# Performance work log

Measured on AMD Instinct MI355X. Metric: run time of the kernel, lower is better.

The kernel has to match this reference:

```python
import jax, jax.numpy as jnp
import numpy as np

N_NODES = 100000
INPUT_DIM = 512
OUTPUT_DIM = 128
N_EDGES = 300000


def setup_inputs() -> dict:
    key = jax.random.key(0)
    k1, k2, k3, k4, k5 = jax.random.split(key, 5)
    x = jax.random.normal(k1, (N_NODES, INPUT_DIM), dtype=jnp.float32)
    train_edges = jax.random.randint(k2, (N_EDGES, 2), 0, N_NODES, dtype=jnp.int64)
    train_false_edges = jax.random.randint(k3, (N_EDGES, 2), 0, N_NODES, dtype=jnp.int64)
    # learned params (xavier / kaiming init approximated with uniform fan-based scales)
    limit_w = float(np.sqrt(6.0 / (INPUT_DIM + OUTPUT_DIM)))
    weight = jax.random.uniform(k4, (INPUT_DIM, OUTPUT_DIM), dtype=jnp.float32,
                                minval=-limit_w, maxval=limit_w)
    limit_w3 = float(np.sqrt(6.0 / OUTPUT_DIM) / np.sqrt(2.0))
    weight_three = jax.random.uniform(k5, (OUTPUT_DIM, 1), dtype=jnp.float32,
                                      minval=-limit_w3, maxval=limit_w3)
    return {"x": x, "train_edges": train_edges, "train_false_edges": train_false_edges,
            "weight": weight, "weight_three": weight_three}


def _decode(z, edges, weight_three):
    # gather endpoints, elementwise multiply, matvec against weight_three
    prod = z[edges[:, 0]] * z[edges[:, 1]]  # [E, output_dim]
    return prod @ weight_three               # [E, 1]


def reference(x, train_edges, train_false_edges, weight, weight_three):
    z = x @ weight  # encode: [N, output_dim]
    z1 = _decode(z, train_edges, weight_three)
    z2 = _decode(z, train_false_edges, weight_three)
    return jax.nn.sigmoid(jnp.concatenate((z1, z2), axis=0))
```

## Files before the change

kernel.cpp:

```cpp
#include <hip/hip_runtime.h>
#include <math.h>

#define IN_DIM 512
#define OUT_DIM 128
#define BM 64
#define BK 64
#define NKT (IN_DIM / BK)

typedef __attribute__((ext_vector_type(8))) __bf16 bf16x8;
typedef __attribute__((ext_vector_type(4))) float f32x4;

__device__ inline unsigned short f2bf(float f) {
    unsigned u = __float_as_uint(f);
    u += 0x7FFFu + ((u >> 16) & 1u);
    return (unsigned short)(u >> 16);
}
__device__ inline float bf2f(unsigned short h) {
    return __uint_as_float((unsigned)h << 16);
}
__device__ inline unsigned pack2(unsigned short a, unsigned short b) {
    return (unsigned)a | ((unsigned)b << 16);
}

__device__ inline int swz(int row, int kbyte) {
    return row * 128 + (kbyte ^ ((row & 7) << 4));
}

__global__ void wt2_kernel(const float* __restrict__ w, unsigned short* __restrict__ wt2) {
    int idx = blockIdx.x * 256 + threadIdx.x;
    int k = idx >> 7;
    int n = idx & 127;
    wt2[(((k >> 3) * 128) + n) * 8 + (k & 7)] = f2bf(w[idx]);
}

__global__ __launch_bounds__(256, 4) void gemm_mfma(const float* __restrict__ x,
                                                    const unsigned short* __restrict__ wt2,
                                                    unsigned short* __restrict__ zb,
                                                    int M) {
    __shared__ unsigned short sAh[BM * BK];
    __shared__ unsigned short sAl[BM * BK];
    char* const pAh = (char*)sAh;
    char* const pAl = (char*)sAl;

    const int tid  = threadIdx.x;
    const int lane = tid & 63;
    const int wid  = tid >> 6;
    const int wm   = wid >> 1;
    const int wn   = wid & 1;
    const int block_row = blockIdx.x * BM;

    f32x4 acc[2][4];
#pragma unroll
    for (int i = 0; i < 2; ++i)
#pragma unroll
        for (int j = 0; j < 4; ++j) acc[i][j] = (f32x4){0.f, 0.f, 0.f, 0.f};

    const int a_row = tid >> 2;
    const int a_col = (tid & 3) * 16;
    const bool a_ok = (block_row + a_row) < M;
    const float* xp = x + (size_t)(block_row + a_row) * IN_DIM + a_col;
    const int a_b0 = swz(a_row, a_col * 2);
    const int a_b1 = swz(a_row, a_col * 2 + 16);

    const int fr  = lane & 15;
    const int fk4 = lane >> 4;
    const int fkb = fk4 * 16;

    const unsigned short* wtb = wt2 + (size_t)fk4 * 1024 + (wn * 64 + fr) * 8;

    float4 ra[4];
    const float4 z4 = make_float4(0.f, 0.f, 0.f, 0.f);

#pragma unroll
    for (int i = 0; i < 4; ++i) ra[i] = a_ok ? *(const float4*)(xp + 4 * i) : z4;

#pragma unroll
    for (int kt = 0; kt < NKT; ++kt) {
        if (kt) __syncthreads();
        unsigned short h[16], l[16];
        const float* rf = (const float*)ra;
#pragma unroll
        for (int i = 0; i < 16; ++i) {
            h[i] = f2bf(rf[i]);
            l[i] = f2bf(rf[i] - bf2f(h[i]));
        }
        uint4 uh0, uh1, ul0, ul1;
        uh0.x = pack2(h[0], h[1]);  uh0.y = pack2(h[2], h[3]);
        uh0.z = pack2(h[4], h[5]);  uh0.w = pack2(h[6], h[7]);
        uh1.x = pack2(h[8], h[9]);  uh1.y = pack2(h[10], h[11]);
        uh1.z = pack2(h[12], h[13]); uh1.w = pack2(h[14], h[15]);
        ul0.x = pack2(l[0], l[1]);  ul0.y = pack2(l[2], l[3]);
        ul0.z = pack2(l[4], l[5]);  ul0.w = pack2(l[6], l[7]);
        ul1.x = pack2(l[8], l[9]);  ul1.y = pack2(l[10], l[11]);
        ul1.z = pack2(l[12], l[13]); ul1.w = pack2(l[14], l[15]);
        *(uint4*)(pAh + a_b0) = uh0;
        *(uint4*)(pAh + a_b1) = uh1;
        *(uint4*)(pAl + a_b0) = ul0;
        *(uint4*)(pAl + a_b1) = ul1;
        __syncthreads();

        if (kt + 1 < NKT) {
            const int k0 = (kt + 1) * BK;
#pragma unroll
            for (int i = 0; i < 4; ++i)
                ra[i] = a_ok ? *(const float4*)(xp + k0 + 4 * i) : z4;
        }

#pragma unroll
        for (int ks = 0; ks < 2; ++ks) {
            bf16x8 ah[2], al[2], bv[4];
#pragma unroll
            for (int mf = 0; mf < 2; ++mf) {
                ah[mf] = *(const bf16x8*)(pAh + swz(wm * 32 + mf * 16 + fr, ks * 64 + fkb));
                al[mf] = *(const bf16x8*)(pAl + swz(wm * 32 + mf * 16 + fr, ks * 64 + fkb));
            }
#pragma unroll
            for (int nf = 0; nf < 4; ++nf)
                bv[nf] = *(const bf16x8*)(wtb + kt * 8192 + ks * 4096 + nf * 128);
#pragma unroll
            for (int mf = 0; mf < 2; ++mf)
#pragma unroll
                for (int nf = 0; nf < 4; ++nf) {
                    acc[mf][nf] = __builtin_amdgcn_mfma_f32_16x16x32_bf16(
                        ah[mf], bv[nf], acc[mf][nf], 0, 0, 0);
                    acc[mf][nf] = __builtin_amdgcn_mfma_f32_16x16x32_bf16(
                        al[mf], bv[nf], acc[mf][nf], 0, 0, 0);
                }
        }
    }

    const int crow0 = (lane >> 4) * 4;
    const int ccol  = lane & 15;
#pragma unroll
    for (int mf = 0; mf < 2; ++mf)
#pragma unroll
        for (int r = 0; r < 4; ++r) {
            const int grow = block_row + wm * 32 + mf * 16 + crow0 + r;
            if (grow < M) {
                unsigned short* zr = zb + (size_t)grow * OUT_DIM + wn * 64 + ccol;
#pragma unroll
                for (int nf = 0; nf < 4; ++nf)
                    zr[nf * 16] = f2bf(acc[mf][nf][r]);
            }
        }
}

__global__ __launch_bounds__(256) void decode_kernel(const unsigned short* __restrict__ zb,
                                                     const int* __restrict__ e1,
                                                     const int* __restrict__ e2,
                                                     const float* __restrict__ w3,
                                                     float* __restrict__ out,
                                                     int E1, int E2) {
    const int tid  = threadIdx.x;
    const int lane = tid & 63;
    const int sub  = lane & 15;
    const int sg   = lane >> 4;
    const int Etot = E1 + E2;
    const int nquads = (Etot + 3) >> 2;

    float w3r[8];
    *(float4*)&w3r[0] = *(const float4*)(w3 + sub * 8);
    *(float4*)&w3r[4] = *(const float4*)(w3 + sub * 8 + 4);

    const int wave_global = blockIdx.x * 4 + (tid >> 6);
    const int nwaves = gridDim.x * 4;

    for (int q = wave_global; q < nquads; q += nwaves) {
        const int e = q * 4 + sg;
        if (e < Etot) {
            int2 ab;
            if (e < E1) ab = ((const int2*)e1)[e];
            else        ab = ((const int2*)e2)[e - E1];

            const uint4 ua = *(const uint4*)(zb + (size_t)ab.x * OUT_DIM + sub * 8);
            const uint4 ub = *(const uint4*)(zb + (size_t)ab.y * OUT_DIM + sub * 8);
            const unsigned pa[4] = {ua.x, ua.y, ua.z, ua.w};
            const unsigned pb[4] = {ub.x, ub.y, ub.z, ub.w};

            float v = 0.f;
#pragma unroll
            for (int i = 0; i < 4; ++i) {
                const float a0 = __uint_as_float(pa[i] << 16);
                const float a1 = __uint_as_float(pa[i] & 0xFFFF0000u);
                const float b0 = __uint_as_float(pb[i] << 16);
                const float b1 = __uint_as_float(pb[i] & 0xFFFF0000u);
                v = fmaf(a0 * b0, w3r[2 * i], v);
                v = fmaf(a1 * b1, w3r[2 * i + 1], v);
            }

            v += __shfl_xor(v, 8);
            v += __shfl_xor(v, 4);
            v += __shfl_xor(v, 2);
            v += __shfl_xor(v, 1);

            if (sub == 0) out[e] = 1.f / (1.f + __expf(-v));
        }
    }
}

extern "C" void kernel_launch(void* const* d_in, const int* in_sizes, int n_in,
                              void* d_out, int out_size, void* d_ws, size_t ws_size,
                              hipStream_t stream) {
    const float* x  = (const float*)d_in[0];
    const int*   e1 = (const int*)d_in[1];
    const int*   e2 = (const int*)d_in[2];
    const float* w  = (const float*)d_in[3];
    const float* w3 = (const float*)d_in[4];

    float* out = (float*)d_out;

    const int M  = in_sizes[0] / IN_DIM;
    const int E1 = in_sizes[1] / 2;
    const int E2 = in_sizes[2] / 2;

    unsigned short* zbuf = (unsigned short*)d_ws;
    unsigned short* wt2  = zbuf + (size_t)M * OUT_DIM;

    wt2_kernel<<<(IN_DIM * OUT_DIM) / 256, 256, 0, stream>>>(w, wt2);
    gemm_mfma<<<(M + BM - 1) / BM, 256, 0, stream>>>(x, wt2, zbuf, M);
    decode_kernel<<<4096, 256, 0, stream>>>(zbuf, e1, e2, w3, out, E1, E2);
}
```

Before: 102.7 us.

## Drop split-bf16 low part of x in encoder GEMM and pack decode math

```diff
diff --git a/kernel.cpp b/kernel.cpp
--- a/kernel.cpp
+++ b/kernel.cpp
@@ -9,17 +9,15 @@
 
 typedef __attribute__((ext_vector_type(8))) __bf16 bf16x8;
 typedef __attribute__((ext_vector_type(4))) float f32x4;
+typedef __attribute__((ext_vector_type(2))) float f32x2;
 
 __device__ inline unsigned short f2bf(float f) {
     unsigned u = __float_as_uint(f);
     u += 0x7FFFu + ((u >> 16) & 1u);
     return (unsigned short)(u >> 16);
 }
-__device__ inline float bf2f(unsigned short h) {
-    return __uint_as_float((unsigned)h << 16);
-}
-__device__ inline unsigned pack2(unsigned short a, unsigned short b) {
-    return (unsigned)a | ((unsigned)b << 16);
+__device__ inline unsigned pack2f(float a, float b) {
+    return (unsigned)f2bf(a) | ((unsigned)f2bf(b) << 16);
 }
 
 __device__ inline int swz(int row, int kbyte) {
@@ -33,14 +31,12 @@
     wt2[(((k >> 3) * 128) + n) * 8 + (k & 7)] = f2bf(w[idx]);
 }
 
-__global__ __launch_bounds__(256, 4) void gemm_mfma(const float* __restrict__ x,
+__global__ __launch_bounds__(256, 6) void gemm_mfma(const float* __restrict__ x,
                                                     const unsigned short* __restrict__ wt2,
                                                     unsigned short* __restrict__ zb,
                                                     int M) {
-    __shared__ unsigned short sAh[BM * BK];
-    __shared__ unsigned short sAl[BM * BK];
-    char* const pAh = (char*)sAh;
-    char* const pAl = (char*)sAl;
+    __shared__ unsigned short sA[BM * BK];
+    char* const pA = (char*)sA;
 
     const int tid  = threadIdx.x;
     const int lane = tid & 63;
@@ -77,26 +73,14 @@
 #pragma unroll
     for (int kt = 0; kt < NKT; ++kt) {
         if (kt) __syncthreads();
-        unsigned short h[16], l[16];
         const float* rf = (const float*)ra;
-#pragma unroll
-        for (int i = 0; i < 16; ++i) {
-            h[i] = f2bf(rf[i]);
-            l[i] = f2bf(rf[i] - bf2f(h[i]));
-        }
-        uint4 uh0, uh1, ul0, ul1;
-        uh0.x = pack2(h[0], h[1]);  uh0.y = pack2(h[2], h[3]);
-        uh0.z = pack2(h[4], h[5]);  uh0.w = pack2(h[6], h[7]);
-        uh1.x = pack2(h[8], h[9]);  uh1.y = pack2(h[10], h[11]);
-        uh1.z = pack2(h[12], h[13]); uh1.w = pack2(h[14], h[15]);
-        ul0.x = pack2(l[0], l[1]);  ul0.y = pack2(l[2], l[3]);
-        ul0.z = pack2(l[4], l[5]);  ul0.w = pack2(l[6], l[7]);
-        ul1.x = pack2(l[8], l[9]);  ul1.y = pack2(l[10], l[11]);
-        ul1.z = pack2(l[12], l[13]); ul1.w = pack2(l[14], l[15]);
-        *(uint4*)(pAh + a_b0) = uh0;
-        *(uint4*)(pAh + a_b1) = uh1;
-        *(uint4*)(pAl + a_b0) = ul0;
-        *(uint4*)(pAl + a_b1) = ul1;
+        uint4 u0, u1;
+        u0.x = pack2f(rf[0], rf[1]);   u0.y = pack2f(rf[2], rf[3]);
+        u0.z = pack2f(rf[4], rf[5]);   u0.w = pack2f(rf[6], rf[7]);
+        u1.x = pack2f(rf[8], rf[9]);   u1.y = pack2f(rf[10], rf[11]);
+        u1.z = pack2f(rf[12], rf[13]); u1.w = pack2f(rf[14], rf[15]);
+        *(uint4*)(pA + a_b0) = u0;
+        *(uint4*)(pA + a_b1) = u1;
         __syncthreads();
 
         if (kt + 1 < NKT) {
@@ -108,24 +92,19 @@
 
 #pragma unroll
         for (int ks = 0; ks < 2; ++ks) {
-            bf16x8 ah[2], al[2], bv[4];
-#pragma unroll
-            for (int mf = 0; mf < 2; ++mf) {
-                ah[mf] = *(const bf16x8*)(pAh + swz(wm * 32 + mf * 16 + fr, ks * 64 + fkb));
-                al[mf] = *(const bf16x8*)(pAl + swz(wm * 32 + mf * 16 + fr, ks * 64 + fkb));
-            }
+            bf16x8 af[2], bv[4];
+#pragma unroll
+            for (int mf = 0; mf < 2; ++mf)
+                af[mf] = *(const bf16x8*)(pA + swz(wm * 32 + mf * 16 + fr, ks * 64 + fkb));
 #pragma unroll
             for (int nf = 0; nf < 4; ++nf)
                 bv[nf] = *(const bf16x8*)(wtb + kt * 8192 + ks * 4096 + nf * 128);
 #pragma unroll
             for (int mf = 0; mf < 2; ++mf)
 #pragma unroll
-                for (int nf = 0; nf < 4; ++nf) {
+                for (int nf = 0; nf < 4; ++nf)
                     acc[mf][nf] = __builtin_amdgcn_mfma_f32_16x16x32_bf16(
-                        ah[mf], bv[nf], acc[mf][nf], 0, 0, 0);
-                    acc[mf][nf] = __builtin_amdgcn_mfma_f32_16x16x32_bf16(
-                        al[mf], bv[nf], acc[mf][nf], 0, 0, 0);
-                }
+                        af[mf], bv[nf], acc[mf][nf], 0, 0, 0);
         }
     }
 
@@ -158,9 +137,15 @@
     const int Etot = E1 + E2;
     const int nquads = (Etot + 3) >> 2;
 
-    float w3r[8];
-    *(float4*)&w3r[0] = *(const float4*)(w3 + sub * 8);
-    *(float4*)&w3r[4] = *(const float4*)(w3 + sub * 8 + 4);
+    f32x2 w3v[4];
+    {
+        const float4 wlo = *(const float4*)(w3 + sub * 8);
+        const float4 whi = *(const float4*)(w3 + sub * 8 + 4);
+        w3v[0] = (f32x2){wlo.x, wlo.y};
+        w3v[1] = (f32x2){wlo.z, wlo.w};
+        w3v[2] = (f32x2){whi.x, whi.y};
+        w3v[3] = (f32x2){whi.z, whi.w};
+    }
 
     const int wave_global = blockIdx.x * 4 + (tid >> 6);
     const int nwaves = gridDim.x * 4;
@@ -177,16 +162,16 @@
             const unsigned pa[4] = {ua.x, ua.y, ua.z, ua.w};
             const unsigned pb[4] = {ub.x, ub.y, ub.z, ub.w};
 
-            float v = 0.f;
+            f32x2 vv = (f32x2){0.f, 0.f};
 #pragma unroll
             for (int i = 0; i < 4; ++i) {
-                const float a0 = __uint_as_float(pa[i] << 16);
-                const float a1 = __uint_as_float(pa[i] & 0xFFFF0000u);
-                const float b0 = __uint_as_float(pb[i] << 16);
-                const float b1 = __uint_as_float(pb[i] & 0xFFFF0000u);
-                v = fmaf(a0 * b0, w3r[2 * i], v);
-                v = fmaf(a1 * b1, w3r[2 * i + 1], v);
+                f32x2 A = (f32x2){__uint_as_float(pa[i] << 16),
+                                  __uint_as_float(pa[i] & 0xFFFF0000u)};
+                f32x2 B = (f32x2){__uint_as_float(pb[i] << 16),
+                                  __uint_as_float(pb[i] & 0xFFFF0000u)};
+                vv += (A * B) * w3v[i];
             }
+            float v = vv.x + vv.y;
 
             v += __shfl_xor(v, 8);
             v += __shfl_xor(v, 4);
```

Result: faster. 100.3 us (-2.3%).
